# Optimization experiments

Measured on AMD Instinct MI355X. Metric: run time of the kernel, lower is better.

The kernel has to match this reference:

```python
import jax, jax.numpy as jnp
import numpy as np

B, N, E, T, F, D, H, HOR = 2, 5000, 40000, 12, 16, 128, 4, 12
C = D // H
NEG_SLOPE = 0.2   # PyG GATConv leaky_relu slope
LN_EPS = 1e-5


def setup_inputs() -> dict:
    key = jax.random.key(0)
    ks = jax.random.split(key, 12)
    s = 0.05
    def rn(k, shape):
        return jax.random.normal(k, shape, jnp.float32) * s
    return {
        "x": jax.random.normal(ks[0], (B, N, T, F), jnp.float32),
        "edge_index": jax.random.randint(ks[1], (2, E), 0, N),
        "edge_weight": jax.random.uniform(ks[2], (E,), dtype=jnp.float32),
        # GATConv params (lin: F->D, att_src/att_dst/att_edge: [H,C], lin_edge: 1->D)
        "W_lin": rn(ks[3], (F, D)),
        "att_src": rn(ks[4], (H, C)),
        "att_dst": rn(ks[5], (H, C)),
        "W_edge": rn(ks[6], (1, D)),
        "att_edge": rn(ks[7], (H, C)),
        "gat_bias": jnp.zeros((D,), jnp.float32),
        # LSTM (1 layer), PyTorch gate order i,f,g,o
        "W_ih": rn(ks[8], (4 * D, D)),
        "W_hh": rn(ks[9], (4 * D, D)),
        "b_ih": jnp.zeros((4 * D,), jnp.float32),
        "b_hh": jnp.zeros((4 * D,), jnp.float32),
        # head: LayerNorm -> Linear(D,D) -> ReLU -> Linear(D,HOR)
        "ln_g": jnp.ones((D,), jnp.float32),
        "ln_b": jnp.zeros((D,), jnp.float32),
        "W1": rn(ks[10], (D, D)),
        "b1": jnp.zeros((D,), jnp.float32),
        "W2": rn(ks[11], (D, HOR)),
        "b2": jnp.zeros((HOR,), jnp.float32),
    }


def _forward(x, edge_weight, W_lin, att_src, att_dst, W_edge, att_edge, gat_bias,
             W_ih, W_hh, b_ih, b_hh, ln_g, ln_b, W1, b1, W2, b2, edge_index):
    b, n, t, f = x.shape
    h, c = att_src.shape
    d = h * c
    src, dst = edge_index[0], edge_index[1]

    # --- GATConv, vectorized over batch and all timesteps at once ---
    hx = jnp.einsum('bntf,fd->bntd', x, W_lin).reshape(b, n, t, h, c)
    a_src = jnp.einsum('bnthc,hc->bnth', hx, att_src)
    a_dst = jnp.einsum('bnthc,hc->bnth', hx, att_dst)
    e_emb = (edge_weight[:, None] * W_edge[0][None, :]).reshape(-1, h, c)  # [E,H,C]
    a_edge = jnp.einsum('ehc,hc->eh', e_emb, att_edge)                     # [E,H]
    alpha = a_src[:, src] + a_dst[:, dst] + a_edge[None, :, None, :]       # [B,E,T,H]
    alpha = jax.nn.leaky_relu(alpha, NEG_SLOPE)
    alpha = jnp.moveaxis(alpha, 1, 0)                                      # [E,B,T,H]
    # scatter-softmax over edges sharing a destination node
    amax = jax.lax.stop_gradient(jax.ops.segment_max(alpha, dst, num_segments=n))
    ex = jnp.exp(alpha - amax[dst])
    den = jax.ops.segment_sum(ex, dst, num_segments=n)
    att = ex / (den[dst] + 1e-16)                                          # [E,B,T,H]
    msg = jnp.moveaxis(hx[:, src], 1, 0) * att[..., None]                  # [E,B,T,H,C]
    agg = jax.ops.segment_sum(msg, dst, num_segments=n)                    # [N,B,T,H,C]
    gnn = jax.nn.elu(jnp.moveaxis(agg, 0, 1).reshape(b, n, t, d) + gat_bias)

    # --- LSTM over time, batch = B*N ---
    rnn_in = gnn.reshape(b * n, t, d)
    def step(carry, xt):
        hh, cc = carry
        g = xt @ W_ih.T + hh @ W_hh.T + b_ih + b_hh
        i, fg, gg, o = jnp.split(g, 4, axis=-1)
        cc = jax.nn.sigmoid(fg) * cc + jax.nn.sigmoid(i) * jnp.tanh(gg)
        hh = jax.nn.sigmoid(o) * jnp.tanh(cc)
        return (hh, cc), None
    z0 = jnp.zeros((b * n, d), x.dtype)
    (hT, _), _ = jax.lax.scan(step, (z0, z0), jnp.moveaxis(rnn_in, 1, 0))

    # --- head: LayerNorm -> Linear -> ReLU -> Linear (dropout = eval/identity) ---
    mu = hT.mean(-1, keepdims=True)
    var = ((hT - mu) ** 2).mean(-1, keepdims=True)
    ln = (hT - mu) / jnp.sqrt(var + LN_EPS) * ln_g + ln_b
    z = jax.nn.relu(ln @ W1 + b1)
    pred = z @ W2 + b2
    return pred.reshape(b, n, -1)


def reference(x, edge_index, edge_weight, W_lin, att_src, att_dst, W_edge, att_edge,
              gat_bias, W_ih, W_hh, b_ih, b_hh, ln_g, ln_b, W1, b1, W2, b2):
    return _forward(x, edge_weight, W_lin, att_src, att_dst, W_edge, att_edge, gat_bias,
                    W_ih, W_hh, b_ih, b_hh, ln_g, ln_b, W1, b1, W2, b2, edge_index)
```

## Files before the change

### kernel.cpp

```cpp
#include <hip/hip_runtime.h>
#include <math.h>

#define BB  2
#define NN  5000
#define EE  40000
#define TT  12
#define FF  16
#define DD  128
#define HH  4
#define HORZ 12
#define NRT (NN * TT)
#define NTILE (NRT / 16)
#define BPB2 157

typedef short bf16x8 __attribute__((ext_vector_type(8)));
typedef float f32x4  __attribute__((ext_vector_type(4)));

__device__ __forceinline__ float sigfast(float x) {
    return __fdividef(1.f, 1.f + __expf(-x));
}
__device__ __forceinline__ float tanhfast(float x) {
    return __fdividef(2.f, 1.f + __expf(-2.f * x)) - 1.f;
}

__device__ __forceinline__ unsigned short f2bf(float f) {
    unsigned int u = __float_as_uint(f);
    unsigned int r = (u + 0x7fffu + ((u >> 16) & 1u)) >> 16;
    return (unsigned short)r;
}
__device__ __forceinline__ float bf2f(unsigned short h) {
    return __uint_as_float(((unsigned int)h) << 16);
}

__global__ __launch_bounds__(512) void prep_small(
    const float* __restrict__ W_edge, const float* __restrict__ att_edge,
    const float* __restrict__ b_ih, const float* __restrict__ b_hh,
    float* __restrict__ s_h, float* __restrict__ bias_sum)
{
    int tid = threadIdx.x;
    if (tid < 128) {
        float v = W_edge[tid] * att_edge[tid];
        for (int off = 16; off; off >>= 1) v += __shfl_xor(v, off, 32);
        if ((tid & 31) == 0) s_h[tid >> 5] = v;
    }
    bias_sum[tid] = b_ih[tid] + b_hh[tid];
}

__global__ __launch_bounds__(256) void wfrag_kernel(
    const float* __restrict__ W_ih, const float* __restrict__ W_hh,
    unsigned short* __restrict__ WxF, unsigned short* __restrict__ WhF)
{
    int gidx = blockIdx.x * 256 + threadIdx.x;
    if (gidx >= 32 * 4 * 64) return;
    int lane = gidx & 63;
    int ks   = (gidx >> 6) & 3;
    int cg   = gidx >> 8;
    int col  = cg * 16 + (lane & 15);
    #pragma unroll
    for (int j = 0; j < 8; ++j) {
        int k = ks * 32 + (lane >> 4) * 8 + j;
        int o = gidx * 8 + j;
        WxF[o] = f2bf(W_ih[col * DD + k]);
        WhF[o] = f2bf(W_hh[col * DD + k]);
    }
}

__global__ __launch_bounds__(128) void hx_kernel(
    const float* __restrict__ xb, const float* __restrict__ W_lin,
    const float* __restrict__ att_src, const float* __restrict__ att_dst,
    unsigned short* __restrict__ hxb, float* __restrict__ a_srcT,
    float* __restrict__ a_dstT)
{
    const int rt = blockIdx.x;
    const int d  = threadIdx.x;
    const float* xr = xb + (size_t)rt * FF;
    float acc = 0.f;
    #pragma unroll
    for (int f = 0; f < FF; ++f) acc += xr[f] * W_lin[f * DD + d];
    hxb[(size_t)rt * DD + d] = f2bf(acc);
    float vs = acc * att_src[d];
    float vd = acc * att_dst[d];
    for (int off = 16; off; off >>= 1) {
        vs += __shfl_xor(vs, off, 32);
        vd += __shfl_xor(vd, off, 32);
    }
    if ((d & 31) == 0) {
        int h = d >> 5;
        a_srcT[(size_t)rt * HH + h] = vs;
        a_dstT[(size_t)rt * HH + h] = vd;
    }
}

__global__ __launch_bounds__(256) void count_kernel(const int* __restrict__ dst,
                                                    int* __restrict__ counts)
{
    int e = blockIdx.x * 256 + threadIdx.x;
    if (e < EE) atomicAdd(&counts[dst[e]], 1);
}

__global__ __launch_bounds__(1024) void scan_kernel(const int* __restrict__ counts,
                                                    int* __restrict__ offs,
                                                    int* __restrict__ cur)
{
    __shared__ int part[1024];
    const int tid = threadIdx.x;
    const int CH = 5;
    int base = tid * CH;
    int pre[CH];
    int run = 0;
    #pragma unroll
    for (int i = 0; i < CH; ++i) {
        int idx = base + i;
        int v = (idx < NN) ? counts[idx] : 0;
        pre[i] = run;
        run += v;
    }
    part[tid] = run;
    __syncthreads();
    for (int off = 1; off < 1024; off <<= 1) {
        int v = (tid >= off) ? part[tid - off] : 0;
        __syncthreads();
        part[tid] += v;
        __syncthreads();
    }
    int prefix = (tid == 0) ? 0 : part[tid - 1];
    #pragma unroll
    for (int i = 0; i < CH; ++i) {
        int idx = base + i;
        if (idx < NN) {
            int o = prefix + pre[i];
            offs[idx] = o;
            cur[idx]  = o;
        }
    }
    if (tid == 1023) offs[NN] = part[1023];
}

__global__ __launch_bounds__(256) void fill_kernel(const int* __restrict__ dst,
                                                   int* __restrict__ cur,
                                                   int* __restrict__ elist)
{
    int e = blockIdx.x * 256 + threadIdx.x;
    if (e < EE) {
        int p = atomicAdd(&cur[dst[e]], 1);
        elist[p] = e;
    }
}

__global__ __launch_bounds__(128) void gat_kernel(
    const unsigned short* __restrict__ hxb, const float* __restrict__ a_srcT,
    const float* __restrict__ a_dstT, const int* __restrict__ src_arr,
    const float* __restrict__ ew, const float* __restrict__ s_h,
    const int* __restrict__ offs, const int* __restrict__ elist,
    const float* __restrict__ gat_bias, float* __restrict__ gnn)
{
    const int n = blockIdx.x;
    const int d = threadIdx.x;
    const int h = d >> 5;
    const int e0 = offs[n], e1 = offs[n + 1];
    const float sh = s_h[h];
    const float bias = gat_bias[d];

    const size_t base_dst = (size_t)n * TT;
    float ad[TT];
    #pragma unroll
    for (int t = 0; t < TT; ++t) ad[t] = a_dstT[(base_dst + t) * HH + h];

    float den[TT], acc[TT];
    #pragma unroll
    for (int t = 0; t < TT; ++t) { den[t] = 0.f; acc[t] = 0.f; }

    for (int ii = e0; ii < e1; ++ii) {
        int e = elist[ii];
        int s = src_arr[e];
        float aew = ew[e] * sh;
        const size_t base_src = (size_t)s * TT;
        #pragma unroll
        for (int t = 0; t < TT; ++t) {
            float al = a_srcT[(base_src + t) * HH + h] + ad[t] + aew;
            al = (al >= 0.f) ? al : 0.2f * al;
            float exv = __expf(al);
            den[t] += exv;
            acc[t] += exv * bf2f(hxb[(base_src + t) * DD + d]);
        }
    }
    #pragma unroll
    for (int t = 0; t < TT; ++t) {
        float g = acc[t] / (den[t] + 1e-16f) + bias;
        float o = (g > 0.f) ? g : expm1f(g);
        gnn[((size_t)t * NN + n) * DD + d] = o;
    }
}

__global__ __launch_bounds__(512, 2) void gx_gemm(
    const float* __restrict__ gnn,
    const unsigned short* __restrict__ WxF,
    const float* __restrict__ bias_s,
    unsigned short* __restrict__ gxS, float* __restrict__ gxG)
{
    __shared__ unsigned short Ahi[64 * 128];
    __shared__ unsigned short Alo[64 * 128];

    const int tid  = threadIdx.x;
    const int wv   = tid >> 6;
    const int lane = tid & 63;
    const int l15  = lane & 15;
    const int g    = lane >> 4;
    const size_t fr0 = (size_t)blockIdx.x * 64;

    #pragma unroll
    for (int c = 0; c < 2; ++c) {
        int linear = tid + c * 512;
        int row = linear >> 4;
        int k0  = (linear & 15) * 8;
        size_t r = fr0 + row;
        if (r > NRT - 1) r = NRT - 1;
        const float* src = gnn + r * DD + k0;
        float4 v0 = *(const float4*)src;
        float4 v1 = *(const float4*)(src + 4);
        float vv[8] = {v0.x, v0.y, v0.z, v0.w, v1.x, v1.y, v1.z, v1.w};
        bf16x8 h8, l8;
        #pragma unroll
        for (int e = 0; e < 8; ++e) {
            unsigned short hb = f2bf(vv[e]);
            h8[e] = (short)hb;
            l8[e] = (short)f2bf(vv[e] - bf2f(hb));
        }
        int byte = (row * 256 + k0 * 2) ^ ((row & 7) << 4);
        *(bf16x8*)((char*)Ahi + byte) = h8;
        *(bf16x8*)((char*)Alo + byte) = l8;
    }

    bf16x8 wh[16];
    #pragma unroll
    for (int ct = 0; ct < 4; ++ct)
        #pragma unroll
        for (int ks = 0; ks < 4; ++ks) {
            int fidx = (((wv * 4 + ct) * 4 + ks) * 64 + lane) * 8;
            wh[ct * 4 + ks] = *(const bf16x8*)&WxF[fidx];
        }
    #pragma unroll
    for (int i = 0; i < 16; ++i) asm volatile("" : "+v"(wh[i]));
    float bias[4];
    #pragma unroll
    for (int ct = 0; ct < 4; ++ct) bias[ct] = bias_s[(wv * 4 + ct) * 16 + l15];

    __syncthreads();

    #pragma unroll
    for (int ar = 0; ar < 4; ++ar) {
        size_t tile = (size_t)blockIdx.x * 4 + ar;
        if (tile >= NTILE) break;
        bf16x8 ah[4], al[4];
        int row = ar * 16 + l15;
        #pragma unroll
        for (int ks = 0; ks < 4; ++ks) {
            int byte = (row * 256 + (ks * 32 + g * 8) * 2) ^ ((row & 7) << 4);
            ah[ks] = *(const bf16x8*)((const char*)Ahi + byte);
            al[ks] = *(const bf16x8*)((const char*)Alo + byte);
        }
        #pragma unroll
        for (int ct = 0; ct < 4; ++ct) {
            int cg = wv * 4 + ct;
            f32x4 a;
            a[0] = bias[ct]; a[1] = bias[ct]; a[2] = bias[ct]; a[3] = bias[ct];
            #pragma unroll
            for (int ks = 0; ks < 4; ++ks) {
                a = __builtin_amdgcn_mfma_f32_16x16x32_bf16(ah[ks], wh[ct * 4 + ks], a, 0, 0, 0);
                a = __builtin_amdgcn_mfma_f32_16x16x32_bf16(al[ks], wh[ct * 4 + ks], a, 0, 0, 0);
            }
            int off = l15 * 16 + g * 4;
            if (cg >= 16 && cg < 24) {
                *(f32x4*)&gxG[(tile * 8 + (cg - 16)) * 256 + off] = a;
            } else {
                int sidx = (cg < 16) ? cg : cg - 8;
                uint2 p;
                p.x = (unsigned)f2bf(a[0]) | ((unsigned)f2bf(a[1]) << 16);
                p.y = (unsigned)f2bf(a[2]) | ((unsigned)f2bf(a[3]) << 16);
                *(uint2*)&gxS[(tile * 24 + sidx) * 256 + off] = p;
            }
        }
    }
}

__global__ __launch_bounds__(512, 2) void lstm_loop(
    const unsigned short* __restrict__ gxS, const float* __restrict__ gxG,
    long sS, long sG,
    const unsigned short* __restrict__ WhF,
    float* __restrict__ hT)
{
    __shared__ unsigned short hb_hi[2][32 * 128];
    __shared__ unsigned short hb_lo[2][32 * 128];

    const int tid  = threadIdx.x;
    const int wv   = tid >> 6;
    const int lane = tid & 63;
    const int l15  = lane & 15;
    const int g    = lane >> 4;
    const int bat  = blockIdx.x / BPB2;
    const int bk   = blockIdx.x - bat * BPB2;
    const int r0   = bk * 32;

    gxS += (size_t)bat * sS;
    gxG += (size_t)bat * sG;

    bf16x8 wh[4][4];
    #pragma unroll
    for (int gt = 0; gt < 4; ++gt)
        #pragma unroll
        for (int ks = 0; ks < 4; ++ks) {
            int cg = gt * 8 + wv;
            wh[gt][ks] = *(const bf16x8*)&WhF[((cg * 4 + ks) * 64 + lane) * 8];
        }
    #pragma unroll
    for (int gt = 0; gt < 4; ++gt)
        #pragma unroll
        for (int ks = 0; ks < 4; ++ks) asm volatile("" : "+v"(wh[gt][ks]));

    int seqq[2];
    #pragma unroll
    for (int rt = 0; rt < 2; ++rt) {
        int s = r0 + rt * 16 + g * 4;
        seqq[rt] = (s > NN - 4) ? (NN - 4) : s;
    }

    float c8[2][4] = {{0.f,0.f,0.f,0.f},{0.f,0.f,0.f,0.f}};
    uint2  cS[2][3];  f32x4 cG[2];
    uint2  nS[2][3];  f32x4 nG[2];

    #pragma unroll
    for (int rt = 0; rt < 2; ++rt) {
        size_t F = (size_t)seqq[rt];
        size_t tile = F >> 4;
        int off = l15 * 16 + (((int)F & 15) >> 2) * 4;
        cS[rt][0] = *(const uint2*)&gxS[(tile * 24 + wv) * 256 + off];
        cS[rt][1] = *(const uint2*)&gxS[(tile * 24 + 8 + wv) * 256 + off];
        cS[rt][2] = *(const uint2*)&gxS[(tile * 24 + 16 + wv) * 256 + off];
        cG[rt]    = *(const f32x4*)&gxG[(tile * 8 + wv) * 256 + off];
    }

    for (int t = 0; t < TT; ++t) {
        if (t < TT - 1) {
            #pragma unroll
            for (int rt = 0; rt < 2; ++rt) {
                size_t F = (size_t)(t + 1) * NN + seqq[rt];
                size_t tile = F >> 4;
                int off = l15 * 16 + (((int)F & 15) >> 2) * 4;
                nS[rt][0] = *(const uint2*)&gxS[(tile * 24 + wv) * 256 + off];
                nS[rt][1] = *(const uint2*)&gxS[(tile * 24 + 8 + wv) * 256 + off];
                nS[rt][2] = *(const uint2*)&gxS[(tile * 24 + 16 + wv) * 256 + off];
                nG[rt]    = *(const f32x4*)&gxG[(tile * 8 + wv) * 256 + off];
            }
        }

        #pragma unroll
        for (int rt = 0; rt < 2; ++rt) {
            f32x4 acc[4];
            #pragma unroll
            for (int s = 0; s < 3; ++s) {
                int gt = (s == 2) ? 3 : s;
                acc[gt][0] = bf2f((unsigned short)(cS[rt][s].x & 0xffff));
                acc[gt][1] = bf2f((unsigned short)(cS[rt][s].x >> 16));
                acc[gt][2] = bf2f((unsigned short)(cS[rt][s].y & 0xffff));
                acc[gt][3] = bf2f((unsigned short)(cS[rt][s].y >> 16));
            }
            acc[2] = cG[rt];

            if (t > 0) {
                const char* rh = (const char*)hb_hi[t & 1];
                const char* rl = (const char*)hb_lo[t & 1];
                #pragma unroll
                for (int ks = 0; ks < 4; ++ks) {
                    int row = rt * 16 + l15;
                    int byte = (row * 256 + (ks * 32 + g * 8) * 2) ^ ((row & 7) << 4);
                    bf16x8 ah = *(const bf16x8*)(rh + byte);
                    bf16x8 al = *(const bf16x8*)(rl + byte);
                    #pragma unroll
                    for (int gt = 0; gt < 4; ++gt) {
                        acc[gt] = __builtin_amdgcn_mfma_f32_16x16x32_bf16(ah, wh[gt][ks], acc[gt], 0, 0, 0);
                        acc[gt] = __builtin_amdgcn_mfma_f32_16x16x32_bf16(al, wh[gt][ks], acc[gt], 0, 0, 0);
                    }
                }
            }

            #pragma unroll
            for (int i = 0; i < 4; ++i) {
                float c = sigfast(acc[1][i]) * c8[rt][i] +
                          sigfast(acc[0][i]) * tanhfast(acc[2][i]);
                c8[rt][i] = c;
                float hv = sigfast(acc[3][i]) * tanhfast(c);
                if (t < TT - 1) {
                    char* whp = (char*)hb_hi[(t + 1) & 1];
                    char* wlp = (char*)hb_lo[(t + 1) & 1];
                    int row = rt * 16 + g * 4 + i;
                    int d   = wv * 16 + l15;
                    unsigned short hb = f2bf(hv);
                    int byte = (row * 256 + d * 2) ^ ((row & 7) << 4);
                    *(unsigned short*)(whp + byte) = hb;
                    *(unsigned short*)(wlp + byte) = f2bf(hv - bf2f(hb));
                } else {
                    int row = r0 + rt * 16 + g * 4 + i;
                    if (row < NN)
                        hT[((size_t)bat * NN + row) * DD + wv * 16 + l15] = hv;
                }
            }
        }

        if (t < TT - 1) {
            __syncthreads();
            #pragma unroll
            for (int rt = 0; rt < 2; ++rt) {
                cS[rt][0] = nS[rt][0]; cS[rt][1] = nS[rt][1]; cS[rt][2] = nS[rt][2];
                cG[rt] = nG[rt];
            }
        }
    }
}

__global__ __launch_bounds__(512, 4) void head_kernel(
    const float* __restrict__ hT,
    const float* __restrict__ ln_g, const float* __restrict__ ln_b,
    const float* __restrict__ W1, const float* __restrict__ b1,
    const float* __restrict__ W2, const float* __restrict__ b2,
    float* __restrict__ out, int nrows)
{
    __shared__ float lnbuf[16 * 128];
    __shared__ float zbuf[16 * 128];

    const int tid = threadIdx.x;
    const int r0  = blockIdx.x * 16;

    {
        const int row    = tid >> 5;
        const int lane32 = tid & 31;
        int gr = r0 + row; if (gr > nrows - 1) gr = nrows - 1;
        float v[4];
        #pragma unroll
        for (int s = 0; s < 4; ++s) v[s] = hT[(size_t)gr * DD + lane32 + s * 32];
        float sum = v[0] + v[1] + v[2] + v[3];
        for (int off = 16; off; off >>= 1) sum += __shfl_xor(sum, off, 32);
        float mu = sum * (1.f / 128.f);
        float var = 0.f;
        #pragma unroll
        for (int s = 0; s < 4; ++s) { float dv = v[s] - mu; var += dv * dv; }
        for (int off = 16; off; off >>= 1) var += __shfl_xor(var, off, 32);
        float rstd = rsqrtf(var * (1.f / 128.f) + 1e-5f);
        #pragma unroll
        for (int s = 0; s < 4; ++s) {
            int d = lane32 + s * 32;
            lnbuf[row * 128 + d] = (v[s] - mu) * rstd * ln_g[d] + ln_b[d];
        }
    }
    __syncthreads();

    {
        float zv[4];
        #pragma unroll
        for (int s = 0; s < 4; ++s) {
            int lin = tid + s * 512;
            int r2 = lin >> 7, j = lin & 127;
            float a = b1[j];
            #pragma unroll 4
            for (int k = 0; k < 128; ++k) a += lnbuf[r2 * 128 + k] * W1[k * 128 + j];
            zv[s] = fmaxf(a, 0.f);
        }
        #pragma unroll
        for (int s = 0; s < 4; ++s) zbuf[tid + s * 512] = zv[s];
    }
    __syncthreads();

    if (tid < 16 * HORZ) {
        int r2 = tid / HORZ, o = tid % HORZ;
        if (r0 + r2 < nrows) {
            float a = b2[o];
            #pragma unroll 4
            for (int k = 0; k < 128; ++k) a += zbuf[r2 * 128 + k] * W2[k * HORZ + o];
            out[(size_t)(r0 + r2) * HORZ + o] = a;
        }
    }
}

extern "C" void kernel_launch(void* const* d_in, const int* in_sizes, int n_in,
                              void* d_out, int out_size, void* d_ws, size_t ws_size,
                              hipStream_t stream)
{
    const float* x        = (const float*)d_in[0];
    const int*   eidx     = (const int*)d_in[1];
    const float* ew       = (const float*)d_in[2];
    const float* W_lin    = (const float*)d_in[3];
    const float* att_src  = (const float*)d_in[4];
    const float* att_dst  = (const float*)d_in[5];
    const float* W_edge   = (const float*)d_in[6];
    const float* att_edge = (const float*)d_in[7];
    const float* gat_bias = (const float*)d_in[8];
    const float* W_ih     = (const float*)d_in[9];
    const float* W_hh     = (const float*)d_in[10];
    const float* b_ih     = (const float*)d_in[11];
    const float* b_hh     = (const float*)d_in[12];
    const float* ln_g     = (const float*)d_in[13];
    const float* ln_b     = (const float*)d_in[14];
    const float* W1       = (const float*)d_in[15];
    const float* b1       = (const float*)d_in[16];
    const float* W2       = (const float*)d_in[17];
    const float* b2       = (const float*)d_in[18];
    float* out = (float*)d_out;

    char* base = (char*)d_ws;
    float* gnn2            = (float*)base;
    char*  gxb             = base + 30720000;
    unsigned short* gx0S   = (unsigned short*)gxb;
    float*          gx0G   = (float*)(gxb + 46080000);
    unsigned short* gx1S   = (unsigned short*)(gxb + 76800000);
    float*          gx1G   = (float*)(gxb + 76800000 + 46080000);
    char*  tail2           = gxb + 2 * 76800000;
    const long SSTRIDE = 76800000 / 2;
    const long GSTRIDE = 76800000 / 4;

    float* gnn1            = (float*)base;
    float* gxG1            = gnn1 + 7680000;
    unsigned short* gxS1   = (unsigned short*)(gxG1 + 7680000);
    char*  tail1           = (char*)(gxS1 + 23040000);

    size_t tail_bytes = (240000 + 240000 + 512 + 16) * 4 + 2 * 65536 * 2 +
                        (NN + (NN + 8) + NN + EE + 8) * 4;
    size_t need_dual = (size_t)(tail2 - base) + tail_bytes;
    const int dual = (ws_size >= need_dual) ? 1 : 0;

    float* a_srcT  = (float*)(dual ? tail2 : tail1);
    float* a_dstT  = a_srcT + 240000;
    float* bias_s  = a_dstT + 240000;
    float* s_h     = bias_s + 512;
    unsigned short* WxF = (unsigned short*)(s_h + 16);
    unsigned short* WhF = WxF + 65536;
    int*   counts  = (int*)(WhF + 65536);
    int*   offs    = counts + NN;
    int*   cur     = offs + (NN + 8);
    int*   elist   = cur + NN;

    float* gnn = dual ? gnn2 : gnn1;
    float* hT  = gnn;
    unsigned short* hxb = dual ? gx1S : (unsigned short*)gxG1;

    const int* srcA = eidx;
    const int* dstA = eidx + EE;

    hipMemsetAsync(counts, 0, NN * sizeof(int), stream);
    prep_small<<<1, 512, 0, stream>>>(W_edge, att_edge, b_ih, b_hh, s_h, bias_s);
    wfrag_kernel<<<32, 256, 0, stream>>>(W_ih, W_hh, WxF, WhF);
    count_kernel<<<(EE + 255) / 256, 256, 0, stream>>>(dstA, counts);
    scan_kernel<<<1, 1024, 0, stream>>>(counts, offs, cur);
    fill_kernel<<<(EE + 255) / 256, 256, 0, stream>>>(dstA, cur, elist);

    if (dual) {
        for (int b = 0; b < BB; ++b) {
            const float* xb = x + (size_t)b * NN * TT * FF;
            unsigned short* gxSb = b ? gx1S : gx0S;
            float*          gxGb = b ? gx1G : gx0G;
            hx_kernel<<<NRT, 128, 0, stream>>>(xb, W_lin, att_src, att_dst,
                                               hxb, a_srcT, a_dstT);
            gat_kernel<<<NN, 128, 0, stream>>>(hxb, a_srcT, a_dstT, srcA, ew, s_h,
                                               offs, elist, gat_bias, gnn);
            gx_gemm<<<(NRT + 63) / 64, 512, 0, stream>>>(gnn, WxF, bias_s,
                                                         gxSb, gxGb);
        }
        lstm_loop<<<BB * BPB2, 512, 0, stream>>>(gx0S, gx0G, SSTRIDE, GSTRIDE,
                                                 WhF, hT);
        head_kernel<<<(BB * NN) / 16, 512, 0, stream>>>(hT, ln_g, ln_b,
                                                        W1, b1, W2, b2,
                                                        out, BB * NN);
    } else {
        for (int b = 0; b < BB; ++b) {
            const float* xb = x + (size_t)b * NN * TT * FF;
            float* outb = out + (size_t)b * NN * HORZ;
            hx_kernel<<<NRT, 128, 0, stream>>>(xb, W_lin, att_src, att_dst,
                                               hxb, a_srcT, a_dstT);
            gat_kernel<<<NN, 128, 0, stream>>>(hxb, a_srcT, a_dstT, srcA, ew, s_h,
                                               offs, elist, gat_bias, gnn);
            gx_gemm<<<(NRT + 63) / 64, 512, 0, stream>>>(gnn, WxF, bias_s,
                                                         gxS1, gxG1);
            lstm_loop<<<BPB2, 512, 0, stream>>>(gxS1, gxG1, 0, 0, WhF, hT);
            head_kernel<<<(NN + 15) / 16, 512, 0, stream>>>(hT, ln_g, ln_b,
                                                            W1, b1, W2, b2,
                                                            outb, NN);
        }
    }
}
```

Baseline: 427.3 us.

## Stage LSTM gate inputs via async global-to-LDS loads, bf16 g-gate, 48-row blocks

The LSTM loop now prefetches the next timestep's gate pre-activations straight into shared memory with global_load_lds instead of holding them in registers. It also handles 48 rows per block instead of 32, which reduces the block count. The g gate is now stored in bf16 like the other gates, so gx_gemm writes a single uniform buffer and the workspace shrinks. The GAT kernel is split into two blocks per node, each covering half the timesteps, to raise parallelism. In exchange, it uses more shared memory per block, loses precision on the g gate, and repeats the edge traversal for each half.

```diff
diff --git a/kernel.cpp b/kernel.cpp
--- a/kernel.cpp
+++ b/kernel.cpp
@@ -11,10 +11,14 @@
 #define HORZ 12
 #define NRT (NN * TT)
 #define NTILE (NRT / 16)
-#define BPB2 157
+#define LROWS 48
+#define BPB3 105
+#define THALF 6
 
 typedef short bf16x8 __attribute__((ext_vector_type(8)));
 typedef float f32x4  __attribute__((ext_vector_type(4)));
+typedef __attribute__((address_space(3))) unsigned int lds_u32;
+typedef const __attribute__((address_space(1))) unsigned int glb_u32;
 
 __device__ __forceinline__ float sigfast(float x) {
     return __fdividef(1.f, 1.f + __expf(-x));
@@ -154,7 +158,9 @@
     const int* __restrict__ offs, const int* __restrict__ elist,
     const float* __restrict__ gat_bias, float* __restrict__ gnn)
 {
-    const int n = blockIdx.x;
+    const int bid = blockIdx.x;
+    const int n  = bid >> 1;
+    const int t0 = (bid & 1) * THALF;
     const int d = threadIdx.x;
     const int h = d >> 5;
     const int e0 = offs[n], e1 = offs[n + 1];
@@ -162,33 +168,34 @@
     const float bias = gat_bias[d];
 
     const size_t base_dst = (size_t)n * TT;
-    float ad[TT];
-    #pragma unroll
-    for (int t = 0; t < TT; ++t) ad[t] = a_dstT[(base_dst + t) * HH + h];
-
-    float den[TT], acc[TT];
-    #pragma unroll
-    for (int t = 0; t < TT; ++t) { den[t] = 0.f; acc[t] = 0.f; }
+    float ad[THALF];
+    #pragma unroll
+    for (int tt = 0; tt < THALF; ++tt)
+        ad[tt] = a_dstT[(base_dst + t0 + tt) * HH + h];
+
+    float den[THALF], acc[THALF];
+    #pragma unroll
+    for (int tt = 0; tt < THALF; ++tt) { den[tt] = 0.f; acc[tt] = 0.f; }
 
     for (int ii = e0; ii < e1; ++ii) {
         int e = elist[ii];
         int s = src_arr[e];
         float aew = ew[e] * sh;
-        const size_t base_src = (size_t)s * TT;
-        #pragma unroll
-        for (int t = 0; t < TT; ++t) {
-            float al = a_srcT[(base_src + t) * HH + h] + ad[t] + aew;
+        const size_t base_src = (size_t)s * TT + t0;
+        #pragma unroll
+        for (int tt = 0; tt < THALF; ++tt) {
+            float al = a_srcT[(base_src + tt) * HH + h] + ad[tt] + aew;
             al = (al >= 0.f) ? al : 0.2f * al;
             float exv = __expf(al);
-            den[t] += exv;
-            acc[t] += exv * bf2f(hxb[(base_src + t) * DD + d]);
-        }
-    }
-    #pragma unroll
-    for (int t = 0; t < TT; ++t) {
-        float g = acc[t] / (den[t] + 1e-16f) + bias;
+            den[tt] += exv;
+            acc[tt] += exv * bf2f(hxb[(base_src + tt) * DD + d]);
+        }
+    }
+    #pragma unroll
+    for (int tt = 0; tt < THALF; ++tt) {
+        float g = acc[tt] / (den[tt] + 1e-16f) + bias;
         float o = (g > 0.f) ? g : expm1f(g);
-        gnn[((size_t)t * NN + n) * DD + d] = o;
+        gnn[((size_t)(t0 + tt) * NN + n) * DD + d] = o;
     }
 }
 
@@ -196,7 +203,7 @@
     const float* __restrict__ gnn,
     const unsigned short* __restrict__ WxF,
     const float* __restrict__ bias_s,
-    unsigned short* __restrict__ gxS, float* __restrict__ gxG)
+    unsigned short* __restrict__ gxS)
 {
     __shared__ unsigned short Ahi[64 * 128];
     __shared__ unsigned short Alo[64 * 128];
@@ -270,39 +277,33 @@
                 a = __builtin_amdgcn_mfma_f32_16x16x32_bf16(al[ks], wh[ct * 4 + ks], a, 0, 0, 0);
             }
             int off = l15 * 16 + g * 4;
-            if (cg >= 16 && cg < 24) {
-                *(f32x4*)&gxG[(tile * 8 + (cg - 16)) * 256 + off] = a;
-            } else {
-                int sidx = (cg < 16) ? cg : cg - 8;
-                uint2 p;
-                p.x = (unsigned)f2bf(a[0]) | ((unsigned)f2bf(a[1]) << 16);
-                p.y = (unsigned)f2bf(a[2]) | ((unsigned)f2bf(a[3]) << 16);
-                *(uint2*)&gxS[(tile * 24 + sidx) * 256 + off] = p;
-            }
+            uint2 p;
+            p.x = (unsigned)f2bf(a[0]) | ((unsigned)f2bf(a[1]) << 16);
+            p.y = (unsigned)f2bf(a[2]) | ((unsigned)f2bf(a[3]) << 16);
+            *(uint2*)&gxS[(tile * 32 + cg) * 256 + off] = p;
         }
     }
 }
 
 __global__ __launch_bounds__(512, 2) void lstm_loop(
-    const unsigned short* __restrict__ gxS, const float* __restrict__ gxG,
-    long sS, long sG,
+    const unsigned short* __restrict__ gxS, long sS,
     const unsigned short* __restrict__ WhF,
     float* __restrict__ hT)
 {
-    __shared__ unsigned short hb_hi[2][32 * 128];
-    __shared__ unsigned short hb_lo[2][32 * 128];
+    __shared__ unsigned short hb_hi[2][LROWS * 128];
+    __shared__ unsigned short hb_lo[2][LROWS * 128];
+    __shared__ unsigned int gstage[3][4][2][512];
 
     const int tid  = threadIdx.x;
     const int wv   = tid >> 6;
     const int lane = tid & 63;
     const int l15  = lane & 15;
     const int g    = lane >> 4;
-    const int bat  = blockIdx.x / BPB2;
-    const int bk   = blockIdx.x - bat * BPB2;
-    const int r0   = bk * 32;
+    const int bat  = blockIdx.x / BPB3;
+    const int bk   = blockIdx.x - bat * BPB3;
+    const int r0   = bk * LROWS;
 
     gxS += (size_t)bat * sS;
-    gxG += (size_t)bat * sG;
 
     bf16x8 wh[4][4];
     #pragma unroll
@@ -317,54 +318,64 @@
         #pragma unroll
         for (int ks = 0; ks < 4; ++ks) asm volatile("" : "+v"(wh[gt][ks]));
 
-    int seqq[2];
-    #pragma unroll
-    for (int rt = 0; rt < 2; ++rt) {
+    int seqq[3];
+    #pragma unroll
+    for (int rt = 0; rt < 3; ++rt) {
         int s = r0 + rt * 16 + g * 4;
         seqq[rt] = (s > NN - 4) ? (NN - 4) : s;
     }
 
-    float c8[2][4] = {{0.f,0.f,0.f,0.f},{0.f,0.f,0.f,0.f}};
-    uint2  cS[2][3];  f32x4 cG[2];
-    uint2  nS[2][3];  f32x4 nG[2];
-
-    #pragma unroll
-    for (int rt = 0; rt < 2; ++rt) {
-        size_t F = (size_t)seqq[rt];
-        size_t tile = F >> 4;
-        int off = l15 * 16 + (((int)F & 15) >> 2) * 4;
-        cS[rt][0] = *(const uint2*)&gxS[(tile * 24 + wv) * 256 + off];
-        cS[rt][1] = *(const uint2*)&gxS[(tile * 24 + 8 + wv) * 256 + off];
-        cS[rt][2] = *(const uint2*)&gxS[(tile * 24 + 16 + wv) * 256 + off];
-        cG[rt]    = *(const f32x4*)&gxG[(tile * 8 + wv) * 256 + off];
-    }
+    auto issue_stage = [&](int t) {
+        #pragma unroll
+        for (int rt = 0; rt < 3; ++rt) {
+            size_t F = (size_t)t * NN + seqq[rt];
+            size_t tile = F >> 4;
+            int off = l15 * 16 + ((((int)F) & 15) >> 2) * 4;
+            #pragma unroll
+            for (int gt = 0; gt < 4; ++gt) {
+                const unsigned short* gp = gxS + (tile * 32 + gt * 8 + wv) * 256 + off;
+                __builtin_amdgcn_global_load_lds(
+                    (glb_u32*)(const void*)gp,
+                    (lds_u32*)(void*)&gstage[rt][gt][0][wv * 64], 4, 0, 0);
+                __builtin_amdgcn_global_load_lds(
+                    (glb_u32*)(const void*)(gp + 2),
+                    (lds_u32*)(void*)&gstage[rt][gt][1][wv * 64], 4, 0, 0);
+            }
+        }
+    };
+
+    issue_stage(0);
+    float c12[3][4];
+    #pragma unroll
+    for (int rt = 0; rt < 3; ++rt)
+        #pragma unroll
+        for (int i = 0; i < 4; ++i) c12[rt][i] = 0.f;
+    __syncthreads();
 
     for (int t = 0; t < TT; ++t) {
-        if (t < TT - 1) {
+        unsigned int gv[3][4][2];
+        #pragma unroll
+        for (int rt = 0; rt < 3; ++rt)
             #pragma unroll
-            for (int rt = 0; rt < 2; ++rt) {
-                size_t F = (size_t)(t + 1) * NN + seqq[rt];
-                size_t tile = F >> 4;
-                int off = l15 * 16 + (((int)F & 15) >> 2) * 4;
-                nS[rt][0] = *(const uint2*)&gxS[(tile * 24 + wv) * 256 + off];
-                nS[rt][1] = *(const uint2*)&gxS[(tile * 24 + 8 + wv) * 256 + off];
-                nS[rt][2] = *(const uint2*)&gxS[(tile * 24 + 16 + wv) * 256 + off];
-                nG[rt]    = *(const f32x4*)&gxG[(tile * 8 + wv) * 256 + off];
+            for (int gt = 0; gt < 4; ++gt) {
+                gv[rt][gt][0] = gstage[rt][gt][0][tid];
+                gv[rt][gt][1] = gstage[rt][gt][1][tid];
             }
-        }
-
-        #pragma unroll
-        for (int rt = 0; rt < 2; ++rt) {
+        __builtin_amdgcn_sched_barrier(0);
+        asm volatile("s_waitcnt lgkmcnt(0)" ::: "memory");
+        __builtin_amdgcn_sched_barrier(0);
+        if (t < TT - 1) issue_stage(t + 1);
+
+        #pragma unroll
+        for (int rt = 0; rt < 3; ++rt) {
             f32x4 acc[4];
             #pragma unroll
-            for (int s = 0; s < 3; ++s) {
-                int gt = (s == 2) ? 3 : s;
-                acc[gt][0] = bf2f((unsigned short)(cS[rt][s].x & 0xffff));
-                acc[gt][1] = bf2f((unsigned short)(cS[rt][s].x >> 16));
-                acc[gt][2] = bf2f((unsigned short)(cS[rt][s].y & 0xffff));
-                acc[gt][3] = bf2f((unsigned short)(cS[rt][s].y >> 16));
+            for (int gt = 0; gt < 4; ++gt) {
+                acc[gt][0] = bf2f((unsigned short)(gv[rt][gt][0] & 0xffff));
+                acc[gt][1] = bf2f((unsigned short)(gv[rt][gt][0] >> 16));
+                acc[gt][2] = bf2f((unsigned short)(gv[rt][gt][1] & 0xffff));
+                acc[gt][3] = bf2f((unsigned short)(gv[rt][gt][1] >> 16));
             }
-            acc[2] = cG[rt];
 
             if (t > 0) {
                 const char* rh = (const char*)hb_hi[t & 1];
@@ -385,19 +396,17 @@
 
             #pragma unroll
             for (int i = 0; i < 4; ++i) {
-                float c = sigfast(acc[1][i]) * c8[rt][i] +
+                float c = sigfast(acc[1][i]) * c12[rt][i] +
                           sigfast(acc[0][i]) * tanhfast(acc[2][i]);
-                c8[rt][i] = c;
+                c12[rt][i] = c;
                 float hv = sigfast(acc[3][i]) * tanhfast(c);
                 if (t < TT - 1) {
-                    char* whp = (char*)hb_hi[(t + 1) & 1];
-                    char* wlp = (char*)hb_lo[(t + 1) & 1];
                     int row = rt * 16 + g * 4 + i;
                     int d   = wv * 16 + l15;
                     unsigned short hb = f2bf(hv);
                     int byte = (row * 256 + d * 2) ^ ((row & 7) << 4);
-                    *(unsigned short*)(whp + byte) = hb;
-                    *(unsigned short*)(wlp + byte) = f2bf(hv - bf2f(hb));
+                    *(unsigned short*)((char*)hb_hi[(t + 1) & 1] + byte) = hb;
+                    *(unsigned short*)((char*)hb_lo[(t + 1) & 1] + byte) = f2bf(hv - bf2f(hb));
                 } else {
                     int row = r0 + rt * 16 + g * 4 + i;
                     if (row < NN)
@@ -406,14 +415,7 @@
             }
         }
 
-        if (t < TT - 1) {
-            __syncthreads();
-            #pragma unroll
-            for (int rt = 0; rt < 2; ++rt) {
-                cS[rt][0] = nS[rt][0]; cS[rt][1] = nS[rt][1]; cS[rt][2] = nS[rt][2];
-                cG[rt] = nG[rt];
-            }
-        }
+        if (t < TT - 1) __syncthreads();
     }
 }
 
@@ -505,21 +507,18 @@
     const float* b2       = (const float*)d_in[18];
     float* out = (float*)d_out;
 
+    const size_t GXB = 61440000;
     char* base = (char*)d_ws;
-    float* gnn2            = (float*)base;
-    char*  gxb             = base + 30720000;
-    unsigned short* gx0S   = (unsigned short*)gxb;
-    float*          gx0G   = (float*)(gxb + 46080000);
-    unsigned short* gx1S   = (unsigned short*)(gxb + 76800000);
-    float*          gx1G   = (float*)(gxb + 76800000 + 46080000);
-    char*  tail2           = gxb + 2 * 76800000;
-    const long SSTRIDE = 76800000 / 2;
-    const long GSTRIDE = 76800000 / 4;
-
-    float* gnn1            = (float*)base;
-    float* gxG1            = gnn1 + 7680000;
-    unsigned short* gxS1   = (unsigned short*)(gxG1 + 7680000);
-    char*  tail1           = (char*)(gxS1 + 23040000);
+
+    float* gnn2          = (float*)base;
+    unsigned short* gx0S = (unsigned short*)(base + 30720000);
+    unsigned short* gx1S = (unsigned short*)(base + 30720000 + GXB);
+    char* tail2          = base + 30720000 + 2 * GXB;
+    const long SSTRIDE   = (long)(GXB / 2);
+
+    float* gnn1          = (float*)base;
+    unsigned short* gxS1 = (unsigned short*)(base + 30720000);
+    char* tail1          = base + 30720000 + GXB;
 
     size_t tail_bytes = (240000 + 240000 + 512 + 16) * 4 + 2 * 65536 * 2 +
                         (NN + (NN + 8) + NN + EE + 8) * 4;
@@ -539,7 +538,7 @@
 
     float* gnn = dual ? gnn2 : gnn1;
     float* hT  = gnn;
-    unsigned short* hxb = dual ? gx1S : (unsigned short*)gxG1;
+    unsigned short* hxb = dual ? gx1S : gxS1;
 
     const int* srcA = eidx;
     const int* dstA = eidx + EE;
@@ -555,30 +554,26 @@
         for (int b = 0; b < BB; ++b) {
             const float* xb = x + (size_t)b * NN * TT * FF;
             unsigned short* gxSb = b ? gx1S : gx0S;
-            float*          gxGb = b ? gx1G : gx0G;
             hx_kernel<<<NRT, 128, 0, stream>>>(xb, W_lin, att_src, att_dst,
                                                hxb, a_srcT, a_dstT);
-            gat_kernel<<<NN, 128, 0, stream>>>(hxb, a_srcT, a_dstT, srcA, ew, s_h,
-                                               offs, elist, gat_bias, gnn);
-            gx_gemm<<<(NRT + 63) / 64, 512, 0, stream>>>(gnn, WxF, bias_s,
-                                                         gxSb, gxGb);
-        }
-        lstm_loop<<<BB * BPB2, 512, 0, stream>>>(gx0S, gx0G, SSTRIDE, GSTRIDE,
-                                                 WhF, hT);
-        head_kernel<<<(BB * NN) / 16, 512, 0, stream>>>(hT, ln_g, ln_b,
-                                                        W1, b1, W2, b2,
-                                                        out, BB * NN);
+            gat_kernel<<<NN * 2, 128, 0, stream>>>(hxb, a_srcT, a_dstT, srcA, ew,
+                                                   s_h, offs, elist, gat_bias, gnn);
+            gx_gemm<<<(NRT + 63) / 64, 512, 0, stream>>>(gnn, WxF, bias_s, gxSb);
+        }
+        lstm_loop<<<BB * BPB3, 512, 0, stream>>>(gx0S, SSTRIDE, WhF, hT);
+        head_kernel<<<(BB * NN + 15) / 16, 512, 0, stream>>>(hT, ln_g, ln_b,
+                                                             W1, b1, W2, b2,
+                                                             out, BB * NN);
     } else {
         for (int b = 0; b < BB; ++b) {
             const float* xb = x + (size_t)b * NN * TT * FF;
             float* outb = out + (size_t)b * NN * HORZ;
             hx_kernel<<<NRT, 128, 0, stream>>>(xb, W_lin, att_src, att_dst,
                                                hxb, a_srcT, a_dstT);
-            gat_kernel<<<NN, 128, 0, stream>>>(hxb, a_srcT, a_dstT, srcA, ew, s_h,
-                                               offs, elist, gat_bias, gnn);
-            gx_gemm<<<(NRT + 63) / 64, 512, 0, stream>>>(gnn, WxF, bias_s,
-                                                         gxS1, gxG1);
-            lstm_loop<<<BPB2, 512, 0, stream>>>(gxS1, gxG1, 0, 0, WhF, hT);
+            gat_kernel<<<NN * 2, 128, 0, stream>>>(hxb, a_srcT, a_dstT, srcA, ew,
+                                                   s_h, offs, elist, gat_bias, gnn);
+            gx_gemm<<<(NRT + 63) / 64, 512, 0, stream>>>(gnn, WxF, bias_s, gxS1);
+            lstm_loop<<<BPB3, 512, 0, stream>>>(gxS1, 0, WhF, hT);
             head_kernel<<<(NN + 15) / 16, 512, 0, stream>>>(hT, ln_g, ln_b,
                                                             W1, b1, W2, b2,
                                                             outb, NN);
```

New measurement: 412.1 us. -3.5%, faster.
